# Performance work log

Hardware: AMD Instinct MI355X
Metric: run time of the kernel (lower is better)

## Reference

```python
import math
import jax, jax.numpy as jnp
import numpy as np


def setup_inputs() -> dict:
    key = jax.random.key(0)
    ks = jax.random.split(key, 5)
    B, T, C = 4, 2048, 1024
    H = 16
    s = 0.02
    return {
        "x": jax.random.normal(ks[0], (B, T, C), dtype=jnp.float32),
        "W_attn": jax.random.normal(ks[1], (C, 3 * C), dtype=jnp.float32) * s,
        "b_attn": jax.random.normal(ks[2], (3 * C,), dtype=jnp.float32) * s,
        "W_proj": jax.random.normal(ks[3], (C, C), dtype=jnp.float32) * s,
        "b_proj": jax.random.normal(ks[4], (C,), dtype=jnp.float32) * s,
        "n_head": 16,
    }


def reference(x, W_attn, b_attn, W_proj, b_proj, n_head):
    B, T, C = x.shape
    hd = C // n_head
    qkv = x @ W_attn + b_attn  # (B,T,3C)
    q, k, v = jnp.split(qkv, 3, axis=-1)
    # (B,H,T,hd)
    q = q.reshape(B, T, n_head, hd).transpose(0, 2, 1, 3)
    k = k.reshape(B, T, n_head, hd).transpose(0, 2, 1, 3)
    v = v.reshape(B, T, n_head, hd).transpose(0, 2, 1, 3)
    # ||q-k||^2 = |q|^2 + |k|^2 - 2 q.k  (GEMM form, avoids (B,H,T,T,hd) diff tensor)
    q2 = jnp.sum(q * q, axis=-1)[..., :, None]  # (B,H,T,1)
    k2 = jnp.sum(k * k, axis=-1)[..., None, :]  # (B,H,1,T)
    qk = jnp.einsum("bhqd,bhkd->bhqk", q, k)    # (B,H,T,T)
    sq_l2 = q2 + k2 - 2.0 * qk
    scale = -1.0 / (2.0 * math.sqrt(hd))
    scores = jnp.exp(sq_l2 * scale)
    causal = jnp.tril(jnp.ones((T, T), dtype=bool))  # (T,T)
    scores = jnp.where(causal[None, None, :, :], scores, 0.0)
    y = jnp.einsum("bhqk,bhkd->bhqd", scores, v)  # (B,H,T,hd)
    y = y.transpose(0, 2, 1, 3).reshape(B, T, C)
    return y @ W_proj + b_proj
```

## Files before the change

kernel.cpp:

```cpp
#include <hip/hip_runtime.h>

typedef __bf16 bf16;
typedef __bf16 bf16x8 __attribute__((ext_vector_type(8)));
typedef float floatx4 __attribute__((ext_vector_type(4)));

#define MFMA_BF16(a, b, c) __builtin_amdgcn_mfma_f32_16x16x32_bf16((a), (b), (c), 0, 0, 0)

#define GLOAD_LDS16(gp, lp)                                      \
  __builtin_amdgcn_global_load_lds(                              \
      (const __attribute__((address_space(1))) void*)(gp),       \
      (__attribute__((address_space(3))) void*)(lp), 16, 0, 0)

#define SEQ_T 2048
#define DIM_C 1024
#define HDIM 64
#define MROWS 8192
#define N_QKV 3072

__global__ __launch_bounds__(256) void f32_to_bf16(
    const float* __restrict__ in, bf16* __restrict__ out) {
  const size_t i = ((size_t)blockIdx.x * 256 + threadIdx.x) * 8;
  const float4 f0 = *(const float4*)&in[i];
  const float4 f1 = *(const float4*)&in[i + 4];
  bf16x8 v;
  v[0] = (bf16)f0.x; v[1] = (bf16)f0.y; v[2] = (bf16)f0.z; v[3] = (bf16)f0.w;
  v[4] = (bf16)f1.x; v[5] = (bf16)f1.y; v[6] = (bf16)f1.z; v[7] = (bf16)f1.w;
  *(bf16x8*)&out[i] = v;
}

__global__ __launch_bounds__(256) void transpose_f32_bf16(
    const float* __restrict__ in, bf16* __restrict__ out, int R, int C) {
  __shared__ bf16 tile[32][33];
  const int bx = blockIdx.x * 32, by = blockIdx.y * 32;
  const int tx = threadIdx.x & 31, ty = threadIdx.x >> 5;
  for (int i = 0; i < 32; i += 8)
    tile[ty + i][tx] = (bf16)in[(size_t)(by + ty + i) * C + bx + tx];
  __syncthreads();
  for (int i = 0; i < 32; i += 8)
    out[(size_t)(bx + ty + i) * R + by + tx] = tile[tx][ty + i];
}

template <typename OT>
__global__ __launch_bounds__(256) void gemm_lds(
    const bf16* __restrict__ A,
    const bf16* __restrict__ Bt,
    const float* __restrict__ bias,
    OT* __restrict__ Cout,
    int M, int N, int K) {
  __shared__ __align__(16) bf16 Asl[128 * 64];
  __shared__ __align__(16) bf16 Bsl[128 * 64];
  const int bm = blockIdx.y * 128, bn = blockIdx.x * 128;
  const int tid = threadIdx.x;
  const int wave = tid >> 6, lane = tid & 63;
  const int wm = (wave >> 1) * 64, wn = (wave & 1) * 64;
  const int quad = lane >> 4, l16 = lane & 15;

  const floatx4 zero = {0.f, 0.f, 0.f, 0.f};
  floatx4 acc[4][4];
  for (int i = 0; i < 4; i++)
    for (int j = 0; j < 4; j++) acc[i][j] = zero;

  const bf16 *gA[4], *gB[4];
  bf16 *lA[4], *lB[4];
  for (int i = 0; i < 4; i++) {
    const int s = i * 256 + tid;
    const int row = s >> 3;
    const int c = (s & 7) ^ (row & 7);
    gA[i] = &A[(size_t)(bm + row) * K + c * 8];
    gB[i] = &Bt[(size_t)(bn + row) * K + c * 8];
    lA[i] = &Asl[(i * 256 + wave * 64) * 8];
    lB[i] = &Bsl[(i * 256 + wave * 64) * 8];
  }

  for (int k0 = 0; k0 < K; k0 += 64) {
    for (int i = 0; i < 4; i++) GLOAD_LDS16(gA[i] + k0, lA[i]);
    for (int i = 0; i < 4; i++) GLOAD_LDS16(gB[i] + k0, lB[i]);
    __syncthreads();
    for (int kk = 0; kk < 2; kk++) {
      bf16x8 af[4], bfr[4];
      for (int it = 0; it < 4; it++) {
        const int row = wm + it * 16 + l16;
        const int phys = (kk * 4 + quad) ^ (row & 7);
        af[it] = *(const bf16x8*)&Asl[row * 64 + phys * 8];
      }
      for (int jt = 0; jt < 4; jt++) {
        const int row = wn + jt * 16 + l16;
        const int phys = (kk * 4 + quad) ^ (row & 7);
        bfr[jt] = *(const bf16x8*)&Bsl[row * 64 + phys * 8];
      }
      for (int it = 0; it < 4; it++)
        for (int jt = 0; jt < 4; jt++)
          acc[it][jt] = MFMA_BF16(af[it], bfr[jt], acc[it][jt]);
    }
    __syncthreads();
  }
  for (int jt = 0; jt < 4; jt++) {
    const int col = bn + wn + jt * 16 + l16;
    const float bv = bias[col];
    for (int it = 0; it < 4; it++)
      for (int r = 0; r < 4; r++) {
        const int row = bm + wm + it * 16 + quad * 4 + r;
        Cout[(size_t)row * N + col] = (OT)(acc[it][jt][r] + bv);
      }
  }
}

__global__ __launch_bounds__(256, 4) void attn_kernel(
    const bf16* __restrict__ qkv,
    bf16* __restrict__ y) {
  const int p = blockIdx.x;
  const int bh = blockIdx.y;
  const int bb = bh >> 4, h = bh & 15;
  const int qtA = p, qtB = 31 - p;
  const int tid = threadIdx.x;
  const int wave = tid >> 6, lane = tid & 63;
  const int quad = lane >> 4, l16 = lane & 15;

  __shared__ __align__(16) bf16 Ps[128][72];
  __shared__ __align__(16) bf16 Ks[64][72];
  __shared__ __align__(16) bf16 Vt[64][72];
  __shared__ float q2c[128];

  const size_t rowbase = (size_t)bb * SEQ_T;
  const float c2 = -0.09016844f;
  const float m2c2 = 0.18033688f;

  bf16x8 aq[2][2];
  for (int T = 0; T < 2; T++) {
    const int qt = T ? qtB : qtA;
    const size_t grow = rowbase + qt * 64 + wave * 16 + l16;
    float s = 0.f;
    for (int ks = 0; ks < 2; ks++) {
      aq[T][ks] = *(const bf16x8*)&qkv[grow * N_QKV + h * HDIM + ks * 32 + quad * 8];
      for (int j = 0; j < 8; j++) { const float f = (float)aq[T][ks][j]; s += f * f; }
    }
    s += __shfl_xor(s, 16); s += __shfl_xor(s, 32);
    if (quad == 0) q2c[T * 64 + wave * 16 + l16] = s * c2;
  }

  const floatx4 zero = {0.f, 0.f, 0.f, 0.f};
  floatx4 accy[2][4];
  for (int T = 0; T < 2; T++)
    for (int jt = 0; jt < 4; jt++) accy[T][jt] = zero;

  for (int kt = 0; kt <= qtB; kt++) {
    const bool actA = (kt <= qtA);
    {
      const int r0 = tid >> 3, c8 = (tid & 7) << 3;
      for (int i = 0; i < 2; i++) {
        const int r = r0 + i * 32;
        const size_t gr = rowbase + (size_t)(kt * 64 + r);
        const bf16x8 kv = *(const bf16x8*)&qkv[gr * N_QKV + 1024 + h * HDIM + c8];
        *(bf16x8*)&Ks[r][c8] = kv;
        float s = 0.f;
        for (int j = 0; j < 8; j++) { const float f = (float)kv[j]; s += f * f; }
        s += __shfl_xor(s, 1); s += __shfl_xor(s, 2); s += __shfl_xor(s, 4);
        const float vscale = exp2f(s * c2);
        const bf16x8 vv = *(const bf16x8*)&qkv[gr * N_QKV + 2048 + h * HDIM + c8];
        for (int j = 0; j < 8; j++)
          Vt[c8 + j][r ^ c8] = (bf16)((float)vv[j] * vscale);
      }
    }
    __syncthreads();

    bf16x8 bk[4][2];
    for (int jt = 0; jt < 4; jt++)
      for (int ks = 0; ks < 2; ks++)
        bk[jt][ks] = *(const bf16x8*)&Ks[jt * 16 + l16][ks * 32 + quad * 8];
    floatx4 accs[2][4];
    for (int T = 0; T < 2; T++)
      for (int jt = 0; jt < 4; jt++) accs[T][jt] = zero;
    for (int T = 0; T < 2; T++) {
      if (T == 0 && !actA) continue;
      for (int ks = 0; ks < 2; ks++)
        for (int jt = 0; jt < 4; jt++)
          accs[T][jt] = MFMA_BF16(aq[T][ks], bk[jt][ks], accs[T][jt]);
    }

    for (int T = 0; T < 2; T++) {
      if (T == 0 && !actA) continue;
      const bool diag = (kt == (T == 0 ? qtA : qtB));
      for (int jt = 0; jt < 4; jt++) {
        const int nl = jt * 16 + l16;
        for (int r = 0; r < 4; r++) {
          const int ml = wave * 16 + quad * 4 + r;
          float pe = exp2f(m2c2 * accs[T][jt][r]);
          if (diag && nl > ml) pe = 0.f;
          Ps[T * 64 + ml][nl] = (bf16)pe;
        }
      }
    }

    bf16x8 bv[4][2];
    for (int jt = 0; jt < 4; jt++)
      for (int ks = 0; ks < 2; ks++) {
        const int d = jt * 16 + l16;
        bv[jt][ks] = *(const bf16x8*)&Vt[d][(ks * 32 + quad * 8) ^ (d & 0x38)];
      }
    for (int T = 0; T < 2; T++) {
      if (T == 0 && !actA) continue;
      for (int ks = 0; ks < 2; ks++) {
        const bf16x8 ap =
            *(const bf16x8*)&Ps[T * 64 + wave * 16 + l16][ks * 32 + quad * 8];
        for (int jt = 0; jt < 4; jt++)
          accy[T][jt] = MFMA_BF16(ap, bv[jt][ks], accy[T][jt]);
      }
    }
    __syncthreads();
  }

  for (int T = 0; T < 2; T++) {
    const int qt = (T == 0) ? qtA : qtB;
    float ysc[4];
    for (int r = 0; r < 4; r++)
      ysc[r] = exp2f(q2c[T * 64 + wave * 16 + quad * 4 + r]);
    for (int jt = 0; jt < 4; jt++) {
      const int col = h * HDIM + jt * 16 + l16;
      for (int r = 0; r < 4; r++) {
        const int ml = wave * 16 + quad * 4 + r;
        y[(rowbase + qt * 64 + ml) * DIM_C + col] = (bf16)(accy[T][jt][r] * ysc[r]);
      }
    }
  }
}

extern "C" void kernel_launch(void* const* d_in, const int* in_sizes, int n_in,
                              void* d_out, int out_size, void* d_ws, size_t ws_size,
                              hipStream_t stream) {
  const float* x      = (const float*)d_in[0];
  const float* W_attn = (const float*)d_in[1];
  const float* b_attn = (const float*)d_in[2];
  const float* W_proj = (const float*)d_in[3];
  const float* b_proj = (const float*)d_in[4];
  float* out = (float*)d_out;

  char* ws = (char*)d_ws;
  bf16* qkv = (bf16*)(ws);
  bf16* yb  = (bf16*)(ws + 50331648);
  bf16* WaT = (bf16*)(ws + 67108864);
  bf16* WpT = (bf16*)(ws + 73400320);
  bf16* xb  = yb;

  f32_to_bf16<<<dim3(4096), 256, 0, stream>>>(x, xb);
  transpose_f32_bf16<<<dim3(96, 32), 256, 0, stream>>>(W_attn, WaT, 1024, 3072);
  transpose_f32_bf16<<<dim3(32, 32), 256, 0, stream>>>(W_proj, WpT, 1024, 1024);
  gemm_lds<bf16><<<dim3(24, 64), 256, 0, stream>>>(
      xb, WaT, b_attn, qkv, MROWS, N_QKV, DIM_C);
  attn_kernel<<<dim3(16, 64), 256, 0, stream>>>(qkv, yb);
  gemm_lds<float><<<dim3(8, 64), 256, 0, stream>>>(
      yb, WpT, b_proj, out, MROWS, DIM_C, DIM_C);
}
```

Measured before the change: 303.0 us.

## Load K fragments directly from global, drop K LDS tile, remap blocks per XCD

The K tile is no longer staged through shared memory. Each wave reads its MFMA B-fragments for K directly from global memory, which removes the Ks buffer and one LDS round trip. Less LDS per block allows the occupancy hint to rise from 4 to 5 blocks per CU. The grid becomes 1D and is remapped so the blocks for the same batch-head land on the same XCD, aiming for better L2 reuse of K/V. The trade-off is that K is now loaded redundantly by all four waves as uncoalesced strided global reads.

```diff
diff --git a/kernel.cpp b/kernel.cpp
--- a/kernel.cpp
+++ b/kernel.cpp
@@ -105,11 +105,14 @@
   }
 }
 
-__global__ __launch_bounds__(256, 4) void attn_kernel(
+__global__ __launch_bounds__(256, 5) void attn_kernel(
     const bf16* __restrict__ qkv,
     bf16* __restrict__ y) {
-  const int p = blockIdx.x;
-  const int bh = blockIdx.y;
+  const int L = blockIdx.x;
+  const int xcd = L & 7;
+  const int m = L >> 3;
+  const int bh = xcd * 8 + (m & 7);
+  const int p = m >> 3;
   const int bb = bh >> 4, h = bh & 15;
   const int qtA = p, qtB = 31 - p;
   const int tid = threadIdx.x;
@@ -117,7 +120,6 @@
   const int quad = lane >> 4, l16 = lane & 15;
 
   __shared__ __align__(16) bf16 Ps[128][72];
-  __shared__ __align__(16) bf16 Ks[64][72];
   __shared__ __align__(16) bf16 Vt[64][72];
   __shared__ float q2c[128];
 
@@ -151,7 +153,6 @@
         const int r = r0 + i * 32;
         const size_t gr = rowbase + (size_t)(kt * 64 + r);
         const bf16x8 kv = *(const bf16x8*)&qkv[gr * N_QKV + 1024 + h * HDIM + c8];
-        *(bf16x8*)&Ks[r][c8] = kv;
         float s = 0.f;
         for (int j = 0; j < 8; j++) { const float f = (float)kv[j]; s += f * f; }
         s += __shfl_xor(s, 1); s += __shfl_xor(s, 2); s += __shfl_xor(s, 4);
@@ -163,18 +164,22 @@
     }
     __syncthreads();
 
-    bf16x8 bk[4][2];
-    for (int jt = 0; jt < 4; jt++)
-      for (int ks = 0; ks < 2; ks++)
-        bk[jt][ks] = *(const bf16x8*)&Ks[jt * 16 + l16][ks * 32 + quad * 8];
     floatx4 accs[2][4];
     for (int T = 0; T < 2; T++)
       for (int jt = 0; jt < 4; jt++) accs[T][jt] = zero;
-    for (int T = 0; T < 2; T++) {
-      if (T == 0 && !actA) continue;
-      for (int ks = 0; ks < 2; ks++)
-        for (int jt = 0; jt < 4; jt++)
-          accs[T][jt] = MFMA_BF16(aq[T][ks], bk[jt][ks], accs[T][jt]);
+    {
+      const bf16* kb =
+          &qkv[(rowbase + (size_t)kt * 64 + l16) * N_QKV + 1024 + h * HDIM + quad * 8];
+      for (int jt = 0; jt < 4; jt++) {
+        const bf16x8 bk0 = *(const bf16x8*)&kb[(size_t)(jt * 16) * N_QKV];
+        const bf16x8 bk1 = *(const bf16x8*)&kb[(size_t)(jt * 16) * N_QKV + 32];
+        if (actA) {
+          accs[0][jt] = MFMA_BF16(aq[0][0], bk0, accs[0][jt]);
+          accs[0][jt] = MFMA_BF16(aq[0][1], bk1, accs[0][jt]);
+        }
+        accs[1][jt] = MFMA_BF16(aq[1][0], bk0, accs[1][jt]);
+        accs[1][jt] = MFMA_BF16(aq[1][1], bk1, accs[1][jt]);
+      }
     }
 
     for (int T = 0; T < 2; T++) {
@@ -246,7 +251,7 @@
   transpose_f32_bf16<<<dim3(32, 32), 256, 0, stream>>>(W_proj, WpT, 1024, 1024);
   gemm_lds<bf16><<<dim3(24, 64), 256, 0, stream>>>(
       xb, WaT, b_attn, qkv, MROWS, N_QKV, DIM_C);
-  attn_kernel<<<dim3(16, 64), 256, 0, stream>>>(qkv, yb);
+  attn_kernel<<<dim3(1024), 256, 0, stream>>>(qkv, yb);
   gemm_lds<float><<<dim3(8, 64), 256, 0, stream>>>(
       yb, WpT, b_proj, out, MROWS, DIM_C, DIM_C);
 }
```

New measurement: 386.2 us. +27.5%, slower.
